# Optimization experiments

Hardware: AMD Instinct MI355X
Metric: run time of the kernel (lower is better)

## Reference

```python
import jax, jax.numpy as jnp
import numpy as np

GC_LAMBDA = 0.5   # smoothness weight from __init__
N_SWEEPS = 30     # fixed checkerboard ICM sweeps (each sweep = 2 half-updates)
EPS = 1e-6


def setup_inputs() -> dict:
    key = jax.random.key(0)
    probs = jax.random.uniform(key, (1, 4096, 4096), dtype=jnp.float32)
    return {"probs": probs}


def _nbr_sum(x):
    # sum of 4-connected neighbors with zero padding at the border
    p = jnp.pad(x, 1)
    return p[:-2, 1:-1] + p[2:, 1:-1] + p[1:-1, :-2] + p[1:-1, 2:]


def reference(probs) -> jnp.ndarray:
    """Graph-cut style binarization of a probability map.

    Minimizes the Potts energy
        E(y) = sum_i [ -y_i log p_i - (1-y_i) log(1-p_i) ]
               + lambda * sum_{(i,j) in 4-nbrs} [y_i != y_j]
    The original custom op solves this exactly via min-cut/max-flow; here we
    use the standard fully-vectorized checkerboard ICM relaxation of the same
    energy (fixed number of sweeps, jit-friendly, deterministic).
    """
    p = probs[0]                                   # [H, W]
    u1 = -jnp.log(p + EPS)                         # unary cost of label 1
    u0 = -jnp.log1p(-(p - EPS))                    # unary cost of label 0
    H, W = p.shape
    ncnt = _nbr_sum(jnp.ones((H, W), p.dtype))     # neighbor counts (2/3/4)
    ii = jnp.arange(H)[:, None]
    jj = jnp.arange(W)[None, :]
    parity_map = ((ii + jj) % 2).astype(jnp.int32)  # checkerboard coloring

    labels0 = (p > 0.5).astype(p.dtype)            # init from thresholding

    def half_sweep(labels, parity):
        ns = _nbr_sum(labels)                      # neighbors labeled 1
        cost1 = u1 + GC_LAMBDA * (ncnt - ns)       # disagree with 0-neighbors
        cost0 = u0 + GC_LAMBDA * ns                # disagree with 1-neighbors
        new = (cost1 < cost0).astype(labels.dtype)
        upd = parity_map == parity
        return jnp.where(upd, new, labels), None

    parities = jnp.tile(jnp.array([0, 1], jnp.int32), N_SWEEPS)
    labels, _ = jax.lax.scan(half_sweep, labels0, parities)
    return jnp.expand_dims(labels, axis=0)         # [1, H, W]
```

## Files before the change

### kernel.cpp

```cpp
#include <hip/hip_runtime.h>
#include <math.h>

#define HH 4096
#define WW 4096
#define WPR 64
#define NWORDS (HH * WPR)
typedef unsigned long long u64;

#define TILE_R 128
#define HALO_R 60
#define REG_R  248
#define REG_WC 10
#define RWORDS (REG_R * REG_WC)
#define NTHR   1024
#define WPT    3
#define NSWEEP 60
#define PACK_WPW 8

__device__ __forceinline__ bool decision(float p, int ncnt, int ns) {
    double pd = (double)p;
    double u1 = -log(pd + 1e-6);
    double u0 = -log1p(-(pd - 1e-6));
    double cost1 = u1 + 0.5 * (double)(ncnt - ns);
    double cost0 = u0 + 0.5 * (double)ns;
    return cost1 < cost0;
}

__global__ void setup_kernel(float* __restrict__ C) {
    int t = threadIdx.x;
    if (t >= 15) return;
    int ncnt = 2 + t / 5;
    int ns = t % 5;
    unsigned lo = 0u, hi = 0x3F800000u;
    for (int it = 0; it < 32 && hi - lo > 1; ++it) {
        unsigned mid = lo + (hi - lo) / 2;
        if (decision(__uint_as_float(mid), ncnt, ns)) hi = mid; else lo = mid;
    }
    C[t] = __uint_as_float(hi);
}

__global__ __launch_bounds__(256)
void pack_kernel(const float* __restrict__ probs, const float* __restrict__ C,
                 u64* __restrict__ L, u64* __restrict__ K0,
                 u64* __restrict__ K1, u64* __restrict__ K2) {
    int gwave = (blockIdx.x * 256 + threadIdx.x) >> 6;
    int lane = threadIdx.x & 63;
    int w0 = gwave * PACK_WPW;
    float p[PACK_WPW];
#pragma unroll
    for (int q = 0; q < PACK_WPW; ++q)
        p[q] = probs[((size_t)(w0 + q) << 6) + lane];
    const float c0 = C[10], c1 = C[11], c2 = C[12], c3 = C[13], c4 = C[14];
#pragma unroll
    for (int q = 0; q < PACK_WPW; ++q) {
        int w = w0 + q;
        int i = w >> 6;
        int jbase = (w & 63) << 6;
        float pp = p[q];
        int k = (pp < c0) + (pp < c1) + (pp < c2) + (pp < c3) + (pp < c4);
        bool gE0 = (i == 0), gE1 = (i == HH - 1);
        bool jE0 = (jbase == 0) & (lane == 0);
        bool jE1 = (jbase == WW - 64) & (lane == 63);
        if (gE0 | gE1 | jE0 | jE1) {
            int ncnt = 4 - gE0 - gE1 - jE0 - jE1;
            const float* Cr = C + (ncnt - 2) * 5;
            k = (pp < Cr[0]) + (pp < Cr[1]) + (pp < Cr[2]) + (pp < Cr[3]) + (pp < Cr[4]);
        }
        u64 lb = __ballot(pp > 0.5f);
        u64 b0 = __ballot(k & 1);
        u64 b1 = __ballot(k & 2);
        u64 b2 = __ballot(k & 4);
        if (lane == 0)      L[w]  = lb;
        else if (lane == 1) K0[w] = b0;
        else if (lane == 2) K1[w] = b1;
        else if (lane == 3) K2[w] = b2;
    }
}

__global__ __attribute__((amdgpu_flat_work_group_size(NTHR, NTHR),
                          amdgpu_waves_per_eu(4, 4)))
void fused_all(const u64* __restrict__ Lg, const u64* __restrict__ K0g,
               const u64* __restrict__ K1g, const u64* __restrict__ K2g,
               float* __restrict__ out) {
    __shared__ u64 SL[RWORDS];
    __shared__ int chg[3];

    const int tid = threadIdx.x;
    const int lane = tid & 63;
    const int tr = blockIdx.x >> 3;
    const int tc = blockIdx.x & 7;
    const int r0 = tr * TILE_R - HALO_R;
    const int wc0 = tc * 8 - 1;

    if (tid < 3) chg[tid] = 0;

    u64 cur[WPT], k0[WPT], k1[WPT], k2[WPT], basem[WPT];
    int rr[WPT], cc[WPT];
#pragma unroll
    for (int m = 0; m < WPT; ++m) {
        int idx = tid + NTHR * m;
        int r = 0, c = 0;
        u64 l = 0, a = ~0ull, b = ~0ull, d = ~0ull;
        if (idx < RWORDS) {
            r = idx / REG_WC;
            c = idx - REG_WC * r;
            int g = r0 + r, wc = wc0 + c;
            if (g >= 0 && g < HH && wc >= 0 && wc < WPR) {
                size_t w = (size_t)g * WPR + wc;
                l = Lg[w]; a = K0g[w]; b = K1g[w]; d = K2g[w];
            }
            SL[idx] = l;
        }
        cur[m] = l; k0[m] = a; k1[m] = b; k2[m] = d;
        rr[m] = r; cc[m] = c;
        basem[m] = ((r0 + r) & 1) ? 0xAAAAAAAAAAAAAAAAull
                                  : 0x5555555555555555ull;
    }
    __syncthreads();

    int prevf = 1;
    for (int s = 0; s < NSWEEP; ++s) {
        if (tid == 0) chg[(s + 1) % 3] = 0;
        const u64 flip = (s & 1) ? ~0ull : 0ull;
        const int rlo = s + 1, rhi = REG_R - 1 - s;
        u64 chacc = 0;
#pragma unroll
        for (int m = 0; m < WPT; ++m) {
            int idx = tid + NTHR * m;
            int r = rr[m];
            if (idx < RWORDS && r >= rlo && r < rhi) {
                int c = cc[m];
                u64 center = cur[m];
                u64 up = SL[idx - REG_WC], dn = SL[idx + REG_WC];
                u64 pw = (c > 0) ? SL[idx - 1] : 0ull;
                u64 nw = (c < REG_WC - 1) ? SL[idx + 1] : 0ull;
                u64 lv = (center << 1) | (pw >> 63);
                u64 rv = (center >> 1) | (nw << 63);
                u64 sxy = up ^ dn, ca = up & dn;
                u64 txy = lv ^ rv, cb = lv & rv;
                u64 n0 = sxy ^ txy, cd = sxy & txy;
                u64 n1 = ca ^ cb ^ cd;
                u64 n2 = (ca & cb) | (cd & (ca ^ cb));
                u64 ge = (n2 & ~k2[m]) |
                         (~(n2 ^ k2[m]) & ((n1 & ~k1[m]) |
                                           (~(n1 ^ k1[m]) & (n0 | ~k0[m]))));
                u64 mask = basem[m] ^ flip;
                u64 nv = (ge & mask) | (center & ~mask);
                chacc |= nv ^ center;
                cur[m] = nv;
                SL[idx] = nv;
            }
        }
        if (__ballot(chacc != 0) != 0ull) {
            if (lane == 0) chg[s % 3] = 1;
        }
        __syncthreads();
        int curf = chg[s % 3];
        if (prevf == 0 && curf == 0) break;
        prevf = curf;
    }

#pragma unroll 4
    for (int m = 0; m < 16; ++m) {
        int idx = tid + NTHR * m;
        int ri = idx >> 7;
        int q = idx & 127;
        u64 word = SL[(HALO_R + ri) * REG_WC + 1 + (q >> 4)];
        unsigned bits = (unsigned)(word >> ((q & 15) * 4)) & 0xFu;
        float4 v;
        v.x = (float)(bits & 1u);
        v.y = (float)((bits >> 1) & 1u);
        v.z = (float)((bits >> 2) & 1u);
        v.w = (float)((bits >> 3) & 1u);
        int g = tr * TILE_R + ri;
        ((float4*)out)[(size_t)g * (WW / 4) + (wc0 + 1) * 16 + q] = v;
    }
}

extern "C" void kernel_launch(void* const* d_in, const int* in_sizes, int n_in,
                              void* d_out, int out_size, void* d_ws, size_t ws_size,
                              hipStream_t stream) {
    const float* probs = (const float*)d_in[0];
    float* out = (float*)d_out;
    char* ws = (char*)d_ws;
    float* C = (float*)ws;
    u64* L  = (u64*)(ws + (1u << 20));
    u64* K0 = (u64*)(ws + (3u << 20));
    u64* K1 = (u64*)(ws + (5u << 20));
    u64* K2 = (u64*)(ws + (7u << 20));

    setup_kernel<<<1, 64, 0, stream>>>(C);
    pack_kernel<<<NWORDS / (PACK_WPW * 4), 256, 0, stream>>>(probs, C, L, K0, K1, K2);
    fused_all<<<256, NTHR, 0, stream>>>(L, K0, K1, K2, out);
}
```

Before: 152.7 us.

## Interleave packed label/threshold planes and seed setup bisection analytically

The four separate bit-plane arrays (labels plus three threshold-count bits) are replaced by one interleaved array of 4 words per position. The pack kernel writes each group with one contiguous store, and the main kernel loads it with two 16-byte vector loads instead of four scattered 8-byte loads. Setup now starts its threshold bisection from a closed-form estimate with a narrow bracket, falling back to the full range if the bracket check fails. Each pack wave now also handles 16 words instead of 8.

```diff
diff --git a/kernel.cpp b/kernel.cpp
--- a/kernel.cpp
+++ b/kernel.cpp
@@ -15,7 +15,7 @@
 #define NTHR   1024
 #define WPT    3
 #define NSWEEP 60
-#define PACK_WPW 8
+#define PACK_WPW 16
 
 __device__ __forceinline__ bool decision(float p, int ncnt, int ns) {
     double pd = (double)p;
@@ -31,9 +31,19 @@
     if (t >= 15) return;
     int ncnt = 2 + t / 5;
     int ns = t % 5;
-    unsigned lo = 0u, hi = 0x3F800000u;
-    for (int it = 0; it < 32 && hi - lo > 1; ++it) {
-        unsigned mid = lo + (hi - lo) / 2;
+    double T = 0.5 * (double)(2 * ns - ncnt);
+    double eT = exp(T);
+    double p0 = (1.0 + 1e-6 - 1e-6 * eT) / (1.0 + eT);
+    float f0 = (float)p0;
+    if (f0 < 0.0f) f0 = 0.0f;
+    if (f0 > 1.0f) f0 = 1.0f;
+    unsigned b0 = __float_as_uint(f0);
+    unsigned lo = (b0 > 64u) ? b0 - 64u : 0u;
+    unsigned hi = (b0 + 64u < 0x3F800000u) ? b0 + 64u : 0x3F800000u;
+    if (decision(__uint_as_float(lo), ncnt, ns)) lo = 0u;
+    if (!decision(__uint_as_float(hi), ncnt, ns)) hi = 0x3F800000u;
+    while (hi - lo > 1u) {
+        unsigned mid = lo + (hi - lo) / 2u;
         if (decision(__uint_as_float(mid), ncnt, ns)) hi = mid; else lo = mid;
     }
     C[t] = __uint_as_float(hi);
@@ -41,8 +51,7 @@
 
 __global__ __launch_bounds__(256)
 void pack_kernel(const float* __restrict__ probs, const float* __restrict__ C,
-                 u64* __restrict__ L, u64* __restrict__ K0,
-                 u64* __restrict__ K1, u64* __restrict__ K2) {
+                 u64* __restrict__ Kp) {
     int gwave = (blockIdx.x * 256 + threadIdx.x) >> 6;
     int lane = threadIdx.x & 63;
     int w0 = gwave * PACK_WPW;
@@ -70,18 +79,16 @@
         u64 b0 = __ballot(k & 1);
         u64 b1 = __ballot(k & 2);
         u64 b2 = __ballot(k & 4);
-        if (lane == 0)      L[w]  = lb;
-        else if (lane == 1) K0[w] = b0;
-        else if (lane == 2) K1[w] = b1;
-        else if (lane == 3) K2[w] = b2;
+        if (lane < 4) {
+            u64 v = (lane == 0) ? lb : (lane == 1) ? b0 : (lane == 2) ? b1 : b2;
+            Kp[4ull * w + lane] = v;
+        }
     }
 }
 
 __global__ __attribute__((amdgpu_flat_work_group_size(NTHR, NTHR),
                           amdgpu_waves_per_eu(4, 4)))
-void fused_all(const u64* __restrict__ Lg, const u64* __restrict__ K0g,
-               const u64* __restrict__ K1g, const u64* __restrict__ K2g,
-               float* __restrict__ out) {
+void fused_all(const u64* __restrict__ Kp, float* __restrict__ out) {
     __shared__ u64 SL[RWORDS];
     __shared__ int chg[3];
 
@@ -94,6 +101,7 @@
 
     if (tid < 3) chg[tid] = 0;
 
+    const ulonglong2* Kp2 = (const ulonglong2*)Kp;
     u64 cur[WPT], k0[WPT], k1[WPT], k2[WPT], basem[WPT];
     int rr[WPT], cc[WPT];
 #pragma unroll
@@ -107,7 +115,9 @@
             int g = r0 + r, wc = wc0 + c;
             if (g >= 0 && g < HH && wc >= 0 && wc < WPR) {
                 size_t w = (size_t)g * WPR + wc;
-                l = Lg[w]; a = K0g[w]; b = K1g[w]; d = K2g[w];
+                ulonglong2 x = Kp2[2 * w];
+                ulonglong2 y = Kp2[2 * w + 1];
+                l = x.x; a = x.y; b = y.x; d = y.y;
             }
             SL[idx] = l;
         }
@@ -184,12 +194,9 @@
     float* out = (float*)d_out;
     char* ws = (char*)d_ws;
     float* C = (float*)ws;
-    u64* L  = (u64*)(ws + (1u << 20));
-    u64* K0 = (u64*)(ws + (3u << 20));
-    u64* K1 = (u64*)(ws + (5u << 20));
-    u64* K2 = (u64*)(ws + (7u << 20));
+    u64* Kp = (u64*)(ws + (1u << 20));
 
     setup_kernel<<<1, 64, 0, stream>>>(C);
-    pack_kernel<<<NWORDS / (PACK_WPW * 4), 256, 0, stream>>>(probs, C, L, K0, K1, K2);
-    fused_all<<<256, NTHR, 0, stream>>>(L, K0, K1, K2, out);
-}
+    pack_kernel<<<NWORDS / (PACK_WPW * 4), 256, 0, stream>>>(probs, C, Kp);
+    fused_all<<<256, NTHR, 0, stream>>>(Kp, out);
+}
```

Result: faster. 138.3 us (-9.5%).
